# Kernel optimization log

Hardware: AMD Instinct MI355X
Metric: run time of the kernel (lower is better)

Reference implementation:

```python
import jax, jax.numpy as jnp
import numpy as np

K = 20  # number of nearest neighbors (includes self, distance 0, as in torch topk(largest=False))


def edge_feature(x, k):
    """x: (B, C, N) -> edge features (B, N, k, 2C) = concat[central, neighbor - central]."""
    sq = jnp.sum(x * x, axis=1)                       # (B, N)
    inner = jnp.einsum('bcn,bcm->bnm', x, x)          # (B, N, N)
    d = sq[:, :, None] + sq[:, None, :] - 2.0 * inner # squared pairwise distance
    _, idx = jax.lax.top_k(-d, k)                     # (B, N, k) nearest indices (incl. self)
    xT = jnp.transpose(x, (0, 2, 1))                  # (B, N, C)
    # nb[b,n,j,c] = xT[b, idx[b,n,j], c]
    nb = jnp.take_along_axis(xT[:, :, None, :], idx[:, :, :, None], axis=1)  # (B, N, k, C)
    central = jnp.broadcast_to(xT[:, :, None, :], nb.shape)
    return jnp.concatenate([central, nb - central], axis=-1)  # (B, N, k, 2C)


def setup_inputs() -> dict:
    key = jax.random.key(0)
    ks = jax.random.split(key, 13)
    B, C, N = 8, 3, 4096
    def w(k_, shape, fan_in):
        return (jax.random.normal(k_, shape, dtype=jnp.float32) / np.sqrt(fan_in)).astype(jnp.float32)
    inp = {
        'x':  jax.random.normal(ks[0], (B, C, N), dtype=jnp.float32),
        # local 1x1 conv2d weights (out_ch, in_ch)
        'W1': w(ks[1], (64, 6), 6),        'b1': jnp.zeros((64,), jnp.float32),
        'W2': w(ks[2], (128, 64), 64),     'b2': jnp.zeros((128,), jnp.float32),
        # inter 1x1 conv1d
        'W3': w(ks[3], (1024, 128), 128),  'b3': jnp.zeros((1024,), jnp.float32),
        # global FC
        'W4': w(ks[4], (512, 1024), 1024), 'b4': jnp.zeros((512,), jnp.float32),
        'W5': w(ks[5], (256, 512), 512),   'b5': jnp.zeros((256,), jnp.float32),
        # final linear (torch inits this to zeros -> identity output; use small random for a
        # non-trivial correctness baseline, same math path)
        'W6': 0.01 * w(ks[6], (9, 256), 256), 'b6': jnp.zeros((9,), jnp.float32),
    }
    return inp


def reference(x, W1, b1, W2, b2, W3, b3, W4, b4, W5, b5, W6, b6):
    e = edge_feature(x, K)                                     # (B, N, k, 6)
    h = jax.nn.relu(jnp.einsum('bnkc,oc->bnko', e, W1) + b1)   # (B, N, k, 64)
    h = jax.nn.relu(jnp.einsum('bnkc,oc->bnko', h, W2) + b2)   # (B, N, k, 128)
    h = jnp.max(h, axis=2)                                     # max over k -> (B, N, 128)
    h = jax.nn.relu(jnp.einsum('bnc,oc->bno', h, W3) + b3)     # (B, N, 1024)
    g = jnp.max(h, axis=1)                                     # max over points -> (B, 1024)
    g = jax.nn.relu(g @ W4.T + b4)                             # (B, 512)
    g = jax.nn.relu(g @ W5.T + b5)                             # (B, 256)
    t = g @ W6.T + b6                                          # (B, 9)
    Bsz = x.shape[0]
    out_ch, in_ch = 3, 3
    t = t.reshape(Bsz, out_ch, in_ch) + jnp.eye(out_ch, in_ch, dtype=t.dtype)
    return t
```

## Files before the change

kernel.cpp:

```cpp
#include <hip/hip_runtime.h>
#include <hip/hip_bf16.h>
#include <cstdint>

#define B_SZ 8
#define NPTS 4096
#define KNN  20
#define NTOT (B_SZ * NPTS)
#define PPB  8

typedef unsigned int uint;
typedef unsigned short ushort;
using short8 = __attribute__((ext_vector_type(8))) short;
using f32x4  = __attribute__((ext_vector_type(4))) float;

__device__ __forceinline__ ushort f2bf(float f) {
  uint u = __float_as_uint(f);
  u += 0x7fff + ((u >> 16) & 1);
  return (ushort)(u >> 16);
}
__device__ __forceinline__ float bf2f(ushort h) {
  return __uint_as_float(((uint)h) << 16);
}

__global__ __launch_bounds__(256) void prep_kernel(const float* __restrict__ x,
                                                   const float* __restrict__ W1,
                                                   const float* __restrict__ W3,
                                                   ushort* __restrict__ u,
                                                   ushort* __restrict__ W3b) {
  int blk = blockIdx.x;
  if (blk < 8192) {
    int t = blk * 256 + threadIdx.x;
    int p = t >> 6, o = t & 63;
    int b = p >> 12, n = p & (NPTS - 1);
    const float* xb = x + (size_t)b * 3 * NPTS;
    float x0 = xb[n], x1 = xb[NPTS + n], x2 = xb[2 * NPTS + n];
    const float* w = W1 + o * 6;
    u[t] = f2bf(w[3] * x0 + w[4] * x1 + w[5] * x2);
  } else {
    int t = (blk - 8192) * 256 + threadIdx.x;
    const float4* src = reinterpret_cast<const float4*>(W3 + t * 8);
    float4 f0 = src[0], f1 = src[1];
    uint4 pk;
    pk.x = (uint)f2bf(f0.x) | ((uint)f2bf(f0.y) << 16);
    pk.y = (uint)f2bf(f0.z) | ((uint)f2bf(f0.w) << 16);
    pk.z = (uint)f2bf(f1.x) | ((uint)f2bf(f1.y) << 16);
    pk.w = (uint)f2bf(f1.z) | ((uint)f2bf(f1.w) << 16);
    *reinterpret_cast<uint4*>(W3b + t * 8) = pk;
  }
}

__device__ __forceinline__ void sortf64(float& v, int lane) {
  #pragma unroll
  for (int k = 2; k <= 64; k <<= 1) {
    #pragma unroll
    for (int j = k >> 1; j > 0; j >>= 1) {
      float o = __shfl_xor(v, j, 64);
      bool keepmin = (((lane & k) == 0) == ((lane & j) == 0));
      bool lt = v < o;
      v = (keepmin == lt) ? v : o;
    }
  }
}

__device__ __forceinline__ void sortu64(unsigned long long& v, int lane) {
  #pragma unroll
  for (int k = 2; k <= 64; k <<= 1) {
    #pragma unroll
    for (int j = k >> 1; j > 0; j >>= 1) {
      unsigned long long o = __shfl_xor(v, j, 64);
      bool keepmin = (((lane & k) == 0) == ((lane & j) == 0));
      bool lt = v < o;
      v = (keepmin == lt) ? v : o;
    }
  }
}

__global__ __launch_bounds__(256, 4) void knn_kernel(const float* __restrict__ x,
                                                     int* __restrict__ idx_out) {
  __shared__ int surv[4][256];
  __shared__ int cnt[4];
  const unsigned long long INFK = ~0ull;
  int w = threadIdx.x >> 6, lane = threadIdx.x & 63;
  int row = blockIdx.x * 4 + w;
  int b = row >> 12, n = row & (NPTS - 1);
  const float* xb = x + (size_t)b * 3 * NPTS;
  float qx = xb[n], qy = xb[NPTS + n], qz = xb[2 * NPTS + n];
  if (lane == 0) cnt[w] = 0;

  const float4* X0 = reinterpret_cast<const float4*>(xb);
  const float4* X1 = reinterpret_cast<const float4*>(xb + NPTS);
  const float4* X2 = reinterpret_cast<const float4*>(xb + 2 * NPTS);

  uint kreg[32];
  float bm = 3.0e38f;
  #pragma unroll
  for (int i = 0; i < 16; ++i) {
    int v4 = i * 64 + lane;
    float4 a0 = X0[v4], a1 = X1[v4], a2 = X2[v4];
    float dx, dy, dz, d0, d1, d2, d3;
    dx = a0.x - qx; dy = a1.x - qy; dz = a2.x - qz; d0 = dx*dx + dy*dy + dz*dz;
    dx = a0.y - qx; dy = a1.y - qy; dz = a2.y - qz; d1 = dx*dx + dy*dy + dz*dz;
    dx = a0.z - qx; dy = a1.z - qy; dz = a2.z - qz; d2 = dx*dx + dy*dy + dz*dz;
    dx = a0.w - qx; dy = a1.w - qy; dz = a2.w - qz; d3 = dx*dx + dy*dy + dz*dz;
    bm = fminf(bm, fminf(fminf(d0, d1), fminf(d2, d3)));
    kreg[2*i]   = (__float_as_uint(d0) >> 16) | (__float_as_uint(d1) & 0xFFFF0000u);
    kreg[2*i+1] = (__float_as_uint(d2) >> 16) | (__float_as_uint(d3) & 0xFFFF0000u);
  }

  sortf64(bm, lane);
  float T = __shfl(bm, 19, 64);
  uint T16 = __float_as_uint(T) >> 16;

  asm volatile("s_waitcnt lgkmcnt(0)" ::: "memory");
  #pragma unroll
  for (int i = 0; i < 16; ++i) {
    uint ka = kreg[2*i], kb = kreg[2*i+1];
    int m0 = (i * 64 + lane) * 4;
    if ((ka & 0xffffu) <= T16) { int s = atomicAdd(&cnt[w], 1); if (s < 256) surv[w][s] = m0; }
    if ((ka >> 16)     <= T16) { int s = atomicAdd(&cnt[w], 1); if (s < 256) surv[w][s] = m0 + 1; }
    if ((kb & 0xffffu) <= T16) { int s = atomicAdd(&cnt[w], 1); if (s < 256) surv[w][s] = m0 + 2; }
    if ((kb >> 16)     <= T16) { int s = atomicAdd(&cnt[w], 1); if (s < 256) surv[w][s] = m0 + 3; }
  }
  asm volatile("s_waitcnt lgkmcnt(0)" ::: "memory");
  int M = cnt[w];

  if (M <= 256) {
    unsigned long long run = INFK;
    int nch = (M + 63) >> 6;
    for (int c = 0; c < nch; ++c) {
      int s = c * 64 + lane;
      unsigned long long v = INFK;
      if (s < M) {
        int m = surv[w][s];
        float dx = xb[m] - qx, dy = xb[NPTS + m] - qy, dz = xb[2 * NPTS + m] - qz;
        float d = dx * dx + dy * dy + dz * dz;
        v = ((unsigned long long)__float_as_uint(d) << 32) | (unsigned)m;
      }
      sortu64(v, lane);
      if (c == 0) {
        run = v;
      } else {
        unsigned long long b19 = __shfl(v, (19 - lane) & 63, 64);
        unsigned long long cand = run < b19 ? run : b19;
        run = (lane < KNN) ? cand : INFK;
        sortu64(run, lane);
      }
    }
    if (lane < KNN) idx_out[(size_t)row * KNN + lane] = (int)(run & 0xFFFFFFFFull);
  } else {
    unsigned long long prev = 0ull;
    for (int r = 0; r < KNN; ++r) {
      unsigned long long best = INFK;
      for (int i = 0; i < 16; ++i) {
        int v4 = i * 64 + lane;
        float4 a0 = X0[v4], a1 = X1[v4], a2 = X2[v4];
        float dx, dy, dz, d[4];
        dx = a0.x - qx; dy = a1.x - qy; dz = a2.x - qz; d[0] = dx*dx + dy*dy + dz*dz;
        dx = a0.y - qx; dy = a1.y - qy; dz = a2.y - qz; d[1] = dx*dx + dy*dy + dz*dz;
        dx = a0.z - qx; dy = a1.z - qy; dz = a2.z - qz; d[2] = dx*dx + dy*dy + dz*dz;
        dx = a0.w - qx; dy = a1.w - qy; dz = a2.w - qz; d[3] = dx*dx + dy*dy + dz*dz;
        #pragma unroll
        for (int j = 0; j < 4; ++j) {
          int m = i * 256 + lane * 4 + j;
          unsigned long long key =
              ((unsigned long long)__float_as_uint(d[j]) << 32) | (unsigned)m;
          if ((r == 0 || key > prev) && key < best) best = key;
        }
      }
      #pragma unroll
      for (int off = 32; off; off >>= 1) {
        unsigned long long o = __shfl_xor(best, off, 64);
        best = o < best ? o : best;
      }
      if (lane == 0) idx_out[(size_t)row * KNN + r] = (int)(best & 0xFFFFFFFFull);
      prev = best;
    }
  }
}

__global__ __launch_bounds__(256, 2) void edge_kernel(
    const float* __restrict__ x,  const float* __restrict__ W1, const float* __restrict__ b1,
    const float* __restrict__ W2, const float* __restrict__ b2,
    const ushort* __restrict__ u, const int* __restrict__ idx,
    float* __restrict__ h128) {
  __shared__ __align__(16) char w2s[128 * 128];
  __shared__ __align__(16) char h1s[PPB * 32 * 128];
  __shared__ float vs[PPB * 64];
  __shared__ int   nbs[PPB * KNN];

  int tid = threadIdx.x, w = tid >> 6, l = tid & 63;
  int p0 = blockIdx.x * PPB;
  int b = p0 >> 12;
  const float* xb = x + (size_t)b * 3 * NPTS;

  for (int e = tid; e < 1024; e += 256) {
    int row = e >> 3, c0 = (e & 7) * 8;
    const float* wp = W2 + row * 64 + c0;
    float4 f0 = *(const float4*)wp, f1 = *(const float4*)(wp + 4);
    uint4 pk;
    pk.x = (uint)f2bf(f0.x) | ((uint)f2bf(f0.y) << 16);
    pk.y = (uint)f2bf(f0.z) | ((uint)f2bf(f0.w) << 16);
    pk.z = (uint)f2bf(f1.x) | ((uint)f2bf(f1.y) << 16);
    pk.w = (uint)f2bf(f1.z) | ((uint)f2bf(f1.w) << 16);
    int byte = (row * 128 + c0 * 2) ^ ((row & 7) << 4);
    *(uint4*)(w2s + byte) = pk;
  }
  for (int t = tid; t < PPB * 64; t += 256) {
    int p = t >> 6, c = t & 63;
    int n = (p0 + p) & (NPTS - 1);
    float x0 = xb[n], x1 = xb[NPTS + n], x2 = xb[2 * NPTS + n];
    const float* wr = W1 + c * 6;
    vs[t] = (wr[0] - wr[3]) * x0 + (wr[1] - wr[4]) * x1 + (wr[2] - wr[5]) * x2 + b1[c];
  }
  if (tid < PPB * KNN) nbs[tid] = idx[(size_t)p0 * KNN + tid];
  __syncthreads();

  const ushort* ub = u + (((size_t)b) << 12) * 64;
  #pragma unroll
  for (int j = 0; j < 8; ++j) {
    int e_loc = j * 8 + (l >> 3);
    int p_loc = (w << 1) + (e_loc >> 5);
    int e_in = e_loc & 31;
    int e_src = (e_in < KNN) ? e_in : e_in - KNN;
    int nb = nbs[p_loc * KNN + e_src];
    int c0 = (l & 7) * 8;
    uint4 uv = *(const uint4*)(ub + (((size_t)nb) << 6) + c0);
    const float* vp = vs + p_loc * 64 + c0;
    float4 v0 = *(const float4*)vp, v1 = *(const float4*)(vp + 4);
    float h0 = fmaxf(bf2f((ushort)(uv.x & 0xffff)) + v0.x, 0.f);
    float h1 = fmaxf(bf2f((ushort)(uv.x >> 16))    + v0.y, 0.f);
    float h2 = fmaxf(bf2f((ushort)(uv.y & 0xffff)) + v0.z, 0.f);
    float h3 = fmaxf(bf2f((ushort)(uv.y >> 16))    + v0.w, 0.f);
    float h4 = fmaxf(bf2f((ushort)(uv.z & 0xffff)) + v1.x, 0.f);
    float h5 = fmaxf(bf2f((ushort)(uv.z >> 16))    + v1.y, 0.f);
    float h6 = fmaxf(bf2f((ushort)(uv.w & 0xffff)) + v1.z, 0.f);
    float h7 = fmaxf(bf2f((ushort)(uv.w >> 16))    + v1.w, 0.f);
    uint4 pk;
    pk.x = (uint)f2bf(h0) | ((uint)f2bf(h1) << 16);
    pk.y = (uint)f2bf(h2) | ((uint)f2bf(h3) << 16);
    pk.z = (uint)f2bf(h4) | ((uint)f2bf(h5) << 16);
    pk.w = (uint)f2bf(h6) | ((uint)f2bf(h7) << 16);
    int row = (w << 6) + e_loc;
    int byte = (row * 128 + c0 * 2) ^ ((row & 7) << 4);
    *(uint4*)(h1s + byte) = pk;
  }
  __syncthreads();

  short8 bfr[8][2];
  #pragma unroll
  for (int nt = 0; nt < 8; ++nt) {
    #pragma unroll
    for (int ks = 0; ks < 2; ++ks) {
      int row = nt * 16 + (l & 15);
      int byte = (row * 128 + ks * 64 + (l >> 4) * 16) ^ ((row & 7) << 4);
      bfr[nt][ks] = *(const short8*)(w2s + byte);
    }
  }
  float bias0 = b2[l], bias1 = b2[64 + l];

  #pragma unroll
  for (int pt = 0; pt < 2; ++pt) {
    int rbase = (w << 6) + (pt << 5);
    short8 a[2][2];
    #pragma unroll
    for (int m = 0; m < 2; ++m) {
      #pragma unroll
      for (int ks = 0; ks < 2; ++ks) {
        int row = rbase + m * 16 + (l & 15);
        int byte = (row * 128 + ks * 64 + (l >> 4) * 16) ^ ((row & 7) << 4);
        a[m][ks] = *(const short8*)(h1s + byte);
      }
    }
    float r03 = 0.f, r47 = 0.f;
    #pragma unroll
    for (int nt = 0; nt < 8; ++nt) {
      f32x4 acc0 = {0.f, 0.f, 0.f, 0.f}, acc1 = {0.f, 0.f, 0.f, 0.f};
      acc0 = __builtin_amdgcn_mfma_f32_16x16x32_bf16(a[0][0], bfr[nt][0], acc0, 0, 0, 0);
      acc0 = __builtin_amdgcn_mfma_f32_16x16x32_bf16(a[0][1], bfr[nt][1], acc0, 0, 0, 0);
      acc1 = __builtin_amdgcn_mfma_f32_16x16x32_bf16(a[1][0], bfr[nt][0], acc1, 0, 0, 0);
      acc1 = __builtin_amdgcn_mfma_f32_16x16x32_bf16(a[1][1], bfr[nt][1], acc1, 0, 0, 0);
      float m0 = fmaxf(fmaxf(fmaxf(acc0[0], acc1[0]), fmaxf(acc0[1], acc1[1])),
                       fmaxf(fmaxf(acc0[2], acc1[2]), fmaxf(acc0[3], acc1[3])));
      m0 = fmaxf(m0, __shfl_xor(m0, 16, 64));
      m0 = fmaxf(m0, __shfl_xor(m0, 32, 64));
      if ((l >> 4) == (nt & 3)) { if (nt < 4) r03 = m0; else r47 = m0; }
    }
    int pg = p0 + (w << 1) + pt;
    h128[(size_t)pg * 128 + l]      = fmaxf(r03 + bias0, 0.f);
    h128[(size_t)pg * 128 + 64 + l] = fmaxf(r47 + bias1, 0.f);
  }
}

__global__ __launch_bounds__(256, 2) void inter_kernel(
    const float* __restrict__ h128, const ushort* __restrict__ W3b,
    float* __restrict__ partial) {
  __shared__ __align__(16) char as_[32 * 256];
  int tid = threadIdx.x, w = tid >> 6, l = tid & 63;
  int chunk = blockIdx.x;
  const float* hp = h128 + (size_t)chunk * 32 * 128;

  {
    int row = tid >> 3, c0 = (tid & 7) * 16;
    const float4* src = reinterpret_cast<const float4*>(hp + row * 128 + c0);
    float4 f0 = src[0], f1 = src[1], f2 = src[2], f3 = src[3];
    uint4 p0, p1;
    p0.x = (uint)f2bf(f0.x) | ((uint)f2bf(f0.y) << 16);
    p0.y = (uint)f2bf(f0.z) | ((uint)f2bf(f0.w) << 16);
    p0.z = (uint)f2bf(f1.x) | ((uint)f2bf(f1.y) << 16);
    p0.w = (uint)f2bf(f1.z) | ((uint)f2bf(f1.w) << 16);
    p1.x = (uint)f2bf(f2.x) | ((uint)f2bf(f2.y) << 16);
    p1.y = (uint)f2bf(f2.z) | ((uint)f2bf(f2.w) << 16);
    p1.z = (uint)f2bf(f3.x) | ((uint)f2bf(f3.y) << 16);
    p1.w = (uint)f2bf(f3.z) | ((uint)f2bf(f3.w) << 16);
    int sw = (row & 7) << 4;
    *(uint4*)(as_ + ((row * 256 + c0 * 2) ^ sw))      = p0;
    *(uint4*)(as_ + ((row * 256 + c0 * 2 + 16) ^ sw)) = p1;
  }
  __syncthreads();

  short8 a[2][4];
  #pragma unroll
  for (int m = 0; m < 2; ++m) {
    #pragma unroll
    for (int ks = 0; ks < 4; ++ks) {
      int row = m * 16 + (l & 15);
      int byte = (row * 256 + ks * 64 + (l >> 4) * 16) ^ ((row & 7) << 4);
      a[m][ks] = *(const short8*)(as_ + byte);
    }
  }

  const ushort* wb = W3b + (size_t)(w * 256) * 128;
  float res[4];
  #pragma unroll
  for (int nt = 0; nt < 16; ++nt) {
    f32x4 acc0 = {0.f, 0.f, 0.f, 0.f}, acc1 = {0.f, 0.f, 0.f, 0.f};
    #pragma unroll
    for (int ks = 0; ks < 4; ++ks) {
      short8 bf = *(const short8*)(wb + (size_t)(nt * 16 + (l & 15)) * 128
                                      + ks * 32 + (l >> 4) * 8);
      acc0 = __builtin_amdgcn_mfma_f32_16x16x32_bf16(a[0][ks], bf, acc0, 0, 0, 0);
      acc1 = __builtin_amdgcn_mfma_f32_16x16x32_bf16(a[1][ks], bf, acc1, 0, 0, 0);
    }
    float m0 = fmaxf(fmaxf(fmaxf(acc0[0], acc1[0]), fmaxf(acc0[1], acc1[1])),
                     fmaxf(fmaxf(acc0[2], acc1[2]), fmaxf(acc0[3], acc1[3])));
    m0 = fmaxf(m0, __shfl_xor(m0, 16, 64));
    m0 = fmaxf(m0, __shfl_xor(m0, 32, 64));
    if ((l >> 4) == (nt & 3)) res[nt >> 2] = m0;
  }
  float* pp = partial + (size_t)chunk * 1024 + w * 256;
  #pragma unroll
  for (int g = 0; g < 4; ++g) pp[g * 64 + l] = res[g];
}

__global__ __launch_bounds__(256) void gmax_kernel(const float* __restrict__ partial,
                                                   const float* __restrict__ b3,
                                                   float* __restrict__ g) {
  int t = blockIdx.x * 256 + threadIdx.x;
  if (t >= B_SZ * 1024) return;
  int b = t >> 10, ch = t & 1023;
  const float* p = partial + (size_t)b * 128 * 1024 + ch;
  float m = -3.0e38f;
  for (int i = 0; i < 128; ++i) m = fmaxf(m, p[(size_t)i * 1024]);
  g[t] = fmaxf(m + b3[ch], 0.0f);
}

__global__ __launch_bounds__(64) void fc_kernel(const float* __restrict__ in,
                                                const float* __restrict__ W,
                                                const float* __restrict__ bias,
                                                float* __restrict__ out,
                                                int in_dim, int out_dim, int mode) {
  int blk = blockIdx.x;
  int b = blk / out_dim, o = blk % out_dim;
  int lane = threadIdx.x;
  const float* iv = in + (size_t)b * in_dim;
  const float* w  = W  + (size_t)o * in_dim;
  float s = 0.f;
  for (int c = lane; c < in_dim; c += 64) s += iv[c] * w[c];
  #pragma unroll
  for (int off = 32; off; off >>= 1) s += __shfl_down(s, off);
  if (lane == 0) {
    float r = s + bias[o];
    if (mode == 0) r = fmaxf(r, 0.0f);
    else if (o == 0 || o == 4 || o == 8) r += 1.0f;
    out[blk] = r;
  }
}

extern "C" void kernel_launch(void* const* d_in, const int* in_sizes, int n_in,
                              void* d_out, int out_size, void* d_ws, size_t ws_size,
                              hipStream_t stream) {
  const float* x  = (const float*)d_in[0];
  const float* W1 = (const float*)d_in[1];
  const float* b1 = (const float*)d_in[2];
  const float* W2 = (const float*)d_in[3];
  const float* b2 = (const float*)d_in[4];
  const float* W3 = (const float*)d_in[5];
  const float* b3 = (const float*)d_in[6];
  const float* W4 = (const float*)d_in[7];
  const float* b4 = (const float*)d_in[8];
  const float* W5 = (const float*)d_in[9];
  const float* b5 = (const float*)d_in[10];
  const float* W6 = (const float*)d_in[11];
  const float* b6 = (const float*)d_in[12];
  float* out = (float*)d_out;

  char* ws = (char*)d_ws;
  ushort* u_bf = (ushort*)(ws);
  int*   idxb  = (int*)  (ws + (8u  << 20));
  float* h128  = (float*)(ws + (11u << 20));
  ushort* W3b  = (ushort*)(ws + (27u << 20));
  float* part  = (float*)(ws);
  float* g     = (float*)(ws + (5u  << 20));
  float* g4    = (float*)(ws + (6u  << 20));
  float* g5    = (float*)(ws + (7u  << 20));

  hipLaunchKernelGGL(prep_kernel, dim3(8256), dim3(256), 0, stream, x, W1, W3, u_bf, W3b);
  hipLaunchKernelGGL(knn_kernel,  dim3(8192), dim3(256), 0, stream, x, idxb);
  hipLaunchKernelGGL(edge_kernel, dim3(NTOT / PPB), dim3(256), 0, stream,
                     x, W1, b1, W2, b2, u_bf, idxb, h128);
  hipLaunchKernelGGL(inter_kernel, dim3(1024), dim3(256), 0, stream, h128, W3b, part);
  hipLaunchKernelGGL(gmax_kernel, dim3(32), dim3(256), 0, stream, part, b3, g);
  hipLaunchKernelGGL(fc_kernel, dim3(B_SZ * 512), dim3(64), 0, stream, g,  W4, b4, g4, 1024, 512, 0);
  hipLaunchKernelGGL(fc_kernel, dim3(B_SZ * 256), dim3(64), 0, stream, g4, W5, b5, g5, 512, 256, 0);
  hipLaunchKernelGGL(fc_kernel, dim3(B_SZ * 9),   dim3(64), 0, stream, g5, W6, b6, out, 256, 9, 1);
}
```

Before: 180.0 us.

## Precompute bf16 W2 once and load MFMA B fragments directly from global

Moves the W2 fp32-to-bf16 conversion into the prep kernel so it runs once instead of in each of the 4096 edge blocks. The edge kernel drops its 16KB shared W2 tile and loads its B fragments straight from global memory (L2-resident), issuing those loads before the first barrier. It also raises the launch-bounds occupancy hint from 2 to 4. Separately, the prep kernel packs 8 bf16 u-values per thread with vector stores, which shrinks its grid. The risks are more register pressure under the tighter occupancy hint and scattered global loads for the fragments.

Result: slower. 187.9 us (+4.4%).

```diff
diff --git a/kernel.cpp b/kernel.cpp
--- a/kernel.cpp
+++ b/kernel.cpp
@@ -25,19 +25,29 @@
 __global__ __launch_bounds__(256) void prep_kernel(const float* __restrict__ x,
                                                    const float* __restrict__ W1,
                                                    const float* __restrict__ W3,
+                                                   const float* __restrict__ W2,
                                                    ushort* __restrict__ u,
-                                                   ushort* __restrict__ W3b) {
+                                                   ushort* __restrict__ W3b,
+                                                   ushort* __restrict__ W2b) {
   int blk = blockIdx.x;
-  if (blk < 8192) {
+  if (blk < 1024) {
     int t = blk * 256 + threadIdx.x;
-    int p = t >> 6, o = t & 63;
+    int p = t >> 3, c0 = (t & 7) * 8;
     int b = p >> 12, n = p & (NPTS - 1);
     const float* xb = x + (size_t)b * 3 * NPTS;
     float x0 = xb[n], x1 = xb[NPTS + n], x2 = xb[2 * NPTS + n];
-    const float* w = W1 + o * 6;
-    u[t] = f2bf(w[3] * x0 + w[4] * x1 + w[5] * x2);
-  } else {
-    int t = (blk - 8192) * 256 + threadIdx.x;
+    uint pk[4];
+    #pragma unroll
+    for (int j = 0; j < 8; ++j) {
+      const float* w = W1 + (c0 + j) * 6;
+      float v = w[3] * x0 + w[4] * x1 + w[5] * x2;
+      ushort h = f2bf(v);
+      if (j & 1) pk[j >> 1] |= ((uint)h << 16); else pk[j >> 1] = h;
+    }
+    uint4 q; q.x = pk[0]; q.y = pk[1]; q.z = pk[2]; q.w = pk[3];
+    *reinterpret_cast<uint4*>(u + (size_t)p * 64 + c0) = q;
+  } else if (blk < 1088) {
+    int t = (blk - 1024) * 256 + threadIdx.x;
     const float4* src = reinterpret_cast<const float4*>(W3 + t * 8);
     float4 f0 = src[0], f1 = src[1];
     uint4 pk;
@@ -46,6 +56,16 @@
     pk.z = (uint)f2bf(f1.x) | ((uint)f2bf(f1.y) << 16);
     pk.w = (uint)f2bf(f1.z) | ((uint)f2bf(f1.w) << 16);
     *reinterpret_cast<uint4*>(W3b + t * 8) = pk;
+  } else {
+    int t = (blk - 1088) * 256 + threadIdx.x;
+    const float4* src = reinterpret_cast<const float4*>(W2 + t * 8);
+    float4 f0 = src[0], f1 = src[1];
+    uint4 pk;
+    pk.x = (uint)f2bf(f0.x) | ((uint)f2bf(f0.y) << 16);
+    pk.y = (uint)f2bf(f0.z) | ((uint)f2bf(f0.w) << 16);
+    pk.z = (uint)f2bf(f1.x) | ((uint)f2bf(f1.y) << 16);
+    pk.w = (uint)f2bf(f1.z) | ((uint)f2bf(f1.w) << 16);
+    *reinterpret_cast<uint4*>(W2b + t * 8) = pk;
   }
 }
 
@@ -178,12 +198,11 @@
   }
 }
 
-__global__ __launch_bounds__(256, 2) void edge_kernel(
+__global__ __launch_bounds__(256, 4) void edge_kernel(
     const float* __restrict__ x,  const float* __restrict__ W1, const float* __restrict__ b1,
-    const float* __restrict__ W2, const float* __restrict__ b2,
+    const ushort* __restrict__ W2b, const float* __restrict__ b2,
     const ushort* __restrict__ u, const int* __restrict__ idx,
     float* __restrict__ h128) {
-  __shared__ __align__(16) char w2s[128 * 128];
   __shared__ __align__(16) char h1s[PPB * 32 * 128];
   __shared__ float vs[PPB * 64];
   __shared__ int   nbs[PPB * KNN];
@@ -193,18 +212,6 @@
   int b = p0 >> 12;
   const float* xb = x + (size_t)b * 3 * NPTS;
 
-  for (int e = tid; e < 1024; e += 256) {
-    int row = e >> 3, c0 = (e & 7) * 8;
-    const float* wp = W2 + row * 64 + c0;
-    float4 f0 = *(const float4*)wp, f1 = *(const float4*)(wp + 4);
-    uint4 pk;
-    pk.x = (uint)f2bf(f0.x) | ((uint)f2bf(f0.y) << 16);
-    pk.y = (uint)f2bf(f0.z) | ((uint)f2bf(f0.w) << 16);
-    pk.z = (uint)f2bf(f1.x) | ((uint)f2bf(f1.y) << 16);
-    pk.w = (uint)f2bf(f1.z) | ((uint)f2bf(f1.w) << 16);
-    int byte = (row * 128 + c0 * 2) ^ ((row & 7) << 4);
-    *(uint4*)(w2s + byte) = pk;
-  }
   for (int t = tid; t < PPB * 64; t += 256) {
     int p = t >> 6, c = t & 63;
     int n = (p0 + p) & (NPTS - 1);
@@ -213,6 +220,16 @@
     vs[t] = (wr[0] - wr[3]) * x0 + (wr[1] - wr[4]) * x1 + (wr[2] - wr[5]) * x2 + b1[c];
   }
   if (tid < PPB * KNN) nbs[tid] = idx[(size_t)p0 * KNN + tid];
+
+  short8 bfr[8][2];
+  #pragma unroll
+  for (int nt = 0; nt < 8; ++nt) {
+    #pragma unroll
+    for (int ks = 0; ks < 2; ++ks) {
+      bfr[nt][ks] = *(const short8*)(W2b + (nt * 16 + (l & 15)) * 64
+                                         + ks * 32 + (l >> 4) * 8);
+    }
+  }
   __syncthreads();
 
   const ushort* ub = u + (((size_t)b) << 12) * 64;
@@ -246,16 +263,6 @@
   }
   __syncthreads();
 
-  short8 bfr[8][2];
-  #pragma unroll
-  for (int nt = 0; nt < 8; ++nt) {
-    #pragma unroll
-    for (int ks = 0; ks < 2; ++ks) {
-      int row = nt * 16 + (l & 15);
-      int byte = (row * 128 + ks * 64 + (l >> 4) * 16) ^ ((row & 7) << 4);
-      bfr[nt][ks] = *(const short8*)(w2s + byte);
-    }
-  }
   float bias0 = b2[l], bias1 = b2[64 + l];
 
   #pragma unroll
@@ -409,15 +416,17 @@
   int*   idxb  = (int*)  (ws + (8u  << 20));
   float* h128  = (float*)(ws + (11u << 20));
   ushort* W3b  = (ushort*)(ws + (27u << 20));
+  ushort* W2b  = (ushort*)(ws + (27u << 20) + (256u << 10));
   float* part  = (float*)(ws);
   float* g     = (float*)(ws + (5u  << 20));
   float* g4    = (float*)(ws + (6u  << 20));
   float* g5    = (float*)(ws + (7u  << 20));
 
-  hipLaunchKernelGGL(prep_kernel, dim3(8256), dim3(256), 0, stream, x, W1, W3, u_bf, W3b);
+  hipLaunchKernelGGL(prep_kernel, dim3(1092), dim3(256), 0, stream,
+                     x, W1, W3, W2, u_bf, W3b, W2b);
   hipLaunchKernelGGL(knn_kernel,  dim3(8192), dim3(256), 0, stream, x, idxb);
   hipLaunchKernelGGL(edge_kernel, dim3(NTOT / PPB), dim3(256), 0, stream,
-                     x, W1, b1, W2, b2, u_bf, idxb, h128);
+                     x, W1, b1, W2b, b2, u_bf, idxb, h128);
   hipLaunchKernelGGL(inter_kernel, dim3(1024), dim3(256), 0, stream, h128, W3b, part);
   hipLaunchKernelGGL(gmax_kernel, dim3(32), dim3(256), 0, stream, part, b3, g);
   hipLaunchKernelGGL(fc_kernel, dim3(B_SZ * 512), dim3(64), 0, stream, g,  W4, b4, g4, 1024, 512, 0);
```
